# Performance work log

Measured on AMD Instinct MI355X. Metric: run time of the kernel, lower is better.

Reference implementation:

```python
import jax, jax.numpy as jnp
import numpy as np
from jax import lax

KSIZE = 5  # covariance window size

def _avg_pool_same(x):
    # TF avg_pool2d with SAME padding: zero-pad sums, divide by count of VALID (non-pad) elems
    win = (1, KSIZE, KSIZE, 1)
    s = lax.reduce_window(x, 0.0, lax.add, win, (1, 1, 1, 1), 'SAME')
    cnt = lax.reduce_window(jnp.ones((1, x.shape[1], x.shape[2], 1), x.dtype), 0.0, lax.add, win, (1, 1, 1, 1), 'SAME')
    return s / cnt

def _detect_plane_xz(xyz):
    B, H, W, _ = xyz.shape
    P = _avg_pool_same(xyz)                                   # [B,H,W,3] windowed mean
    xyz2 = (xyz[..., :, None] * xyz[..., None, :]).reshape(B, H, W, 9)
    S = _avg_pool_same(xyz2).reshape(B, H, W, 3, 3)            # windowed second moment
    A = S - P[..., :, None] * P[..., None, :]                  # covariance sigma
    A_max = jnp.max(jnp.abs(A), axis=(-2, -1))
    eval_zero = (A_max < 1e-6).astype(xyz.dtype)
    A = A / jnp.maximum(A_max[..., None, None], 1e-6)
    a00, a11, a22 = A[..., 0, 0], A[..., 1, 1], A[..., 2, 2]
    a01, a02, a12 = A[..., 0, 1], A[..., 0, 2], A[..., 1, 2]
    norm = a01 ** 2 + a02 ** 2 + a12 ** 2
    q = (a00 + a11 + a22) / 3.0
    b00, b11, b22 = a00 - q, a11 - q, a22 - q
    p = jnp.sqrt((b00 ** 2 + b11 ** 2 + b22 ** 2 + 2.0 * norm) / 6.0)
    eig_triple = (p < 1e-6).astype(xyz.dtype) * (1.0 - eval_zero)
    c00 = b11 * b22 - a12 * a12
    c01 = a01 * b22 - a12 * a02
    c02 = a01 * a12 - b11 * a02
    det = (b00 * c00 - a01 * c01 + a02 * c02) / jnp.maximum(p, 1e-6) ** 3
    half_det = jnp.clip(0.5 * det, -1.0, 1.0)
    angle = jnp.arccos(half_det) / 3.0
    beta2 = jnp.cos(angle) * 2.0
    beta0 = jnp.cos(angle + np.pi * 2.0 / 3.0) * 2.0
    beta1 = -(beta0 + beta2)
    betas = jnp.stack([beta0, beta1, beta2], axis=-1)
    evals = q[..., None] + p[..., None] * betas
    evals = (eig_triple * q)[..., None] + ((1.0 - eval_zero) * (1.0 - eig_triple))[..., None] * evals
    eval0, eval1, eval2 = evals[..., 0], evals[..., 1], evals[..., 2]
    denom = jnp.sqrt(jnp.maximum((eval0 - eval1) * (eval0 - eval2), 0.0))
    evec_zero = (denom < 1e-6).astype(xyz.dtype)
    ny_num = jnp.sqrt(jnp.maximum(eval0 ** 2 - (a00 + a22) * eval0 + (a00 * a22 - a02 ** 2), 0.0))
    ny = jnp.clip(ny_num / jnp.maximum(denom, 1e-6), 0.0, 1.0)
    return (1.0 - evec_zero) * ny

def _populate_pcd(depth, K):
    B, H, W, _ = depth.shape
    px, py = jnp.meshgrid(jnp.arange(W, dtype=depth.dtype), jnp.arange(H, dtype=depth.dtype))
    grid = jnp.stack([px, py, jnp.ones_like(px)], axis=-1)   # [H,W,3] homogeneous pixels
    xyz = grid[None] * depth                                 # [B,H,W,3]
    K_inv = jnp.linalg.inv(K)
    return jnp.einsum('bij,bhwj->bhwi', K_inv, xyz)

def setup_inputs():
    key = jax.random.key(0)
    B, H, W = 8, 384, 1280
    disp = jax.random.uniform(key, (B, H, W, 1), jnp.float32, 0.005, 0.3)  # normalized disparity
    K0 = jnp.tile(jnp.array([[720.0, 0.0, W / 2.0], [0.0, 720.0, H / 2.0], [0.0, 0.0, 1.0]], jnp.float32)[None], (B, 1, 1))
    baseline = 0.54 * jnp.ones((B,), jnp.float32)
    return {"disp": disp, "K0": K0, "baseline": baseline, "h0": H, "w0": W}

def reference(disp, K0, baseline, h0, w0):
    B, h1, w1, _ = disp.shape
    rw = float(w1) / float(w0)
    rh = float(h1) / float(h0)
    K_scale = jnp.array([[rw, 0.0, 0.5 * (rw - 1.0)], [0.0, rh, 0.5 * (rh - 1.0)], [0.0, 0.0, 1.0]], jnp.float32)
    K1 = K_scale[None] @ K0
    fxb = K1[:, 0, 0] * baseline
    d = float(w1) * jnp.maximum(disp, 1e-6)
    depth = fxb[:, None, None, None] / d
    xyz = _populate_pcd(depth, K1)
    plane_xz = _detect_plane_xz(xyz)
    cond1 = (xyz[..., 1] > 0.3).astype(jnp.float32)
    cond2 = (plane_xz > 0.85).astype(jnp.float32)
    return depth, cond1 * cond2
```

## Files before the change

### kernel.cpp

```cpp
#include <hip/hip_runtime.h>

#define BATCH 8
#define HH 384
#define WW 1280
#define TW 32
#define TH 16
#define NT (TW * TH)
#define LW (TW + 4)
#define LH (TH + 4)

__device__ __forceinline__ float fast_rcp(float x) {
  float r = __builtin_amdgcn_rcpf(x);
  return fmaf(r, fmaf(-x, r, 1.0f), r);
}
__device__ __forceinline__ float fast_sqrt(float x) {
  return __builtin_amdgcn_sqrtf(x);
}
__device__ __forceinline__ float cos_rev(float r) {
  float d;
  asm("v_cos_f32 %0, %1" : "=v"(d) : "v"(r));
  return d;
}

__global__ void prep_kernel(const float* __restrict__ K0,
                            const float* __restrict__ baseline,
                            const int* __restrict__ h0p,
                            const int* __restrict__ w0p,
                            float* __restrict__ cst) {
  int b = threadIdx.x;
  if (b >= BATCH) return;
  float w0 = (float)w0p[0];
  float h0 = (float)h0p[0];
  float rw = (float)WW / w0;
  float rh = (float)HH / h0;
  float s02 = 0.5f * (rw - 1.0f);
  float s12 = 0.5f * (rh - 1.0f);
  const float* K = K0 + b * 9;
  float k0 = rw * K[0] + s02 * K[6];
  float k1 = rw * K[1] + s02 * K[7];
  float k2 = rw * K[2] + s02 * K[8];
  float k3 = rh * K[3] + s12 * K[6];
  float k4 = rh * K[4] + s12 * K[7];
  float k5 = rh * K[5] + s12 * K[8];
  float k6 = K[6], k7 = K[7], k8 = K[8];
  double a = k0, bb = k1, c = k2, d = k3, e = k4, f = k5, g = k6, h = k7, i = k8;
  double cA = e * i - f * h;
  double cB = -(d * i - f * g);
  double cC = d * h - e * g;
  double det = a * cA + bb * cB + c * cC;
  double idet = 1.0 / det;
  float* o = cst + b * 12;
  o[0] = (float)(cA * idet);
  o[1] = (float)(-(bb * i - c * h) * idet);
  o[2] = (float)((bb * f - c * e) * idet);
  o[3] = (float)(cB * idet);
  o[4] = (float)((a * i - c * g) * idet);
  o[5] = (float)(-(a * f - c * d) * idet);
  o[6] = (float)(cC * idet);
  o[7] = (float)(-(a * h - bb * g) * idet);
  o[8] = (float)((a * e - bb * d) * idet);
  o[9] = k0 * baseline[b];
}

__global__ __launch_bounds__(512) void tmap_fused(
    const float* __restrict__ disp,
    const float* __restrict__ cst,
    float* __restrict__ out_depth,
    float* __restrict__ out_mask) {
  __shared__ float4 tile[LH][LW];
  __shared__ float4 vs0[TH][LW];
  __shared__ float4 vs1[TH][LW];
  __shared__ float  vs2[TH][LW];

  const int b = blockIdx.z;
  const float* C = cst + b * 12;
  const float Ki00 = C[0], Ki01 = C[1], Ki02 = C[2];
  const float Ki10 = C[3], Ki11 = C[4], Ki12 = C[5];
  const float Ki20 = C[6], Ki21 = C[7], Ki22 = C[8];
  const float fxb = C[9];

  const int j0 = blockIdx.x * TW;
  const int i0 = blockIdx.y * TH;
  const int tid = threadIdx.y * TW + threadIdx.x;

  for (int s = tid; s < LH * LW; s += NT) {
    const int ti = s / LW;
    const int tj = s - ti * LW;
    const int gi = i0 - 2 + ti;
    const int gj = j0 - 2 + tj;
    float4 v = make_float4(0.0f, 0.0f, 0.0f, 0.0f);
    if (gi >= 0 && gi < HH && gj >= 0 && gj < WW) {
      const float dsp = disp[(b * HH + gi) * WW + gj];
      const float dd = (float)WW * fmaxf(dsp, 1e-6f);
      const float depth = fxb / dd;
      const float jf = (float)gj;
      const float iff = (float)gi;
      v.x = depth * fmaf(Ki00, jf, fmaf(Ki01, iff, Ki02));
      v.y = depth * fmaf(Ki10, jf, fmaf(Ki11, iff, Ki12));
      v.z = depth * fmaf(Ki20, jf, fmaf(Ki21, iff, Ki22));
      v.w = depth;
    }
    tile[ti][tj] = v;
  }
  __syncthreads();

  for (int s = tid; s < TH * LW; s += NT) {
    const int ti = s / LW;
    const int tj = s - ti * LW;
    float sx = 0.f, sy = 0.f, sz = 0.f;
    float sxx = 0.f, sxy = 0.f, sxz = 0.f, syy = 0.f, syz = 0.f, szz = 0.f;
#pragma unroll
    for (int k = 0; k < 5; ++k) {
      const float4 v = tile[ti + k][tj];
      sx += v.x; sy += v.y; sz += v.z;
      sxx = fmaf(v.x, v.x, sxx);
      sxy = fmaf(v.x, v.y, sxy);
      sxz = fmaf(v.x, v.z, sxz);
      syy = fmaf(v.y, v.y, syy);
      syz = fmaf(v.y, v.z, syz);
      szz = fmaf(v.z, v.z, szz);
    }
    vs0[ti][tj] = make_float4(sx, sy, sz, sxx);
    vs1[ti][tj] = make_float4(sxy, sxz, syy, syz);
    vs2[ti][tj] = szz;
  }
  __syncthreads();

  float s1x = 0.f, s1y = 0.f, s1z = 0.f;
  float m00 = 0.f, m01 = 0.f, m02 = 0.f, m11 = 0.f, m12 = 0.f, m22 = 0.f;
#pragma unroll
  for (int w = 0; w < 5; ++w) {
    const float4 va = vs0[threadIdx.y][threadIdx.x + w];
    const float4 vb = vs1[threadIdx.y][threadIdx.x + w];
    const float vc = vs2[threadIdx.y][threadIdx.x + w];
    s1x += va.x; s1y += va.y; s1z += va.z; m00 += va.w;
    m01 += vb.x; m02 += vb.y; m11 += vb.z; m12 += vb.w;
    m22 += vc;
  }

  const int gi = i0 + threadIdx.y;
  const int gj = j0 + threadIdx.x;
  const int ch = min(gi + 2, HH - 1) - max(gi - 2, 0) + 1;
  const int cw = min(gj + 2, WW - 1) - max(gj - 2, 0) + 1;
  const float cnt = (float)(ch * cw);
  const float rcnt = fast_rcp(cnt);

  const float Px = s1x * rcnt, Py = s1y * rcnt, Pz = s1z * rcnt;
  float a00 = m00 * rcnt - Px * Px;
  float a01 = m01 * rcnt - Px * Py;
  float a02 = m02 * rcnt - Px * Pz;
  float a11 = m11 * rcnt - Py * Py;
  float a12 = m12 * rcnt - Py * Pz;
  float a22 = m22 * rcnt - Pz * Pz;

  float Amax = fmaxf(fabsf(a00), fabsf(a11));
  Amax = fmaxf(Amax, fabsf(a22));
  Amax = fmaxf(Amax, fabsf(a01));
  Amax = fmaxf(Amax, fabsf(a02));
  Amax = fmaxf(Amax, fabsf(a12));
  const float eval_zero = (Amax < 1e-6f) ? 1.0f : 0.0f;
  const float rAm = fast_rcp(fmaxf(Amax, 1e-6f));
  a00 *= rAm; a01 *= rAm; a02 *= rAm; a11 *= rAm; a12 *= rAm; a22 *= rAm;

  const float nrm = a01 * a01 + a02 * a02 + a12 * a12;
  const float q = (a00 + a11 + a22) * (1.0f / 3.0f);
  const float b00 = a00 - q, b11 = a11 - q, b22 = a22 - q;
  const float p =
      fast_sqrt((b00 * b00 + b11 * b11 + b22 * b22 + 2.0f * nrm) * (1.0f / 6.0f));
  const float eig_triple = ((p < 1e-6f) ? 1.0f : 0.0f) * (1.0f - eval_zero);
  const float c00 = b11 * b22 - a12 * a12;
  const float c01 = a01 * b22 - a12 * a02;
  const float c02 = a01 * a12 - b11 * a02;
  const float rpm = fast_rcp(fmaxf(p, 1e-6f));
  const float det = (b00 * c00 - a01 * c01 + a02 * c02) * (rpm * rpm * rpm);
  const float half_det = fminf(fmaxf(0.5f * det, -1.0f), 1.0f);
  const float t = acosf(half_det);
  const float rev = t * 0.05305164769729845f;
  const float beta2 = 2.0f * cos_rev(rev);
  const float beta0 = 2.0f * cos_rev(rev + (1.0f / 3.0f));
  const float beta1 = -(beta0 + beta2);
  float e0 = q + p * beta0;
  float e1 = q + p * beta1;
  float e2 = q + p * beta2;
  const float wsel = (1.0f - eval_zero) * (1.0f - eig_triple);
  e0 = eig_triple * q + wsel * e0;
  e1 = eig_triple * q + wsel * e1;
  e2 = eig_triple * q + wsel * e2;

  const float denom = fast_sqrt(fmaxf((e0 - e1) * (e0 - e2), 0.0f));
  const float evec_zero = (denom < 1e-6f) ? 1.0f : 0.0f;
  const float ny_num =
      fast_sqrt(fmaxf(e0 * e0 - (a00 + a22) * e0 + (a00 * a22 - a02 * a02), 0.0f));
  const float ny =
      fminf(fmaxf(ny_num * fast_rcp(fmaxf(denom, 1e-6f)), 0.0f), 1.0f);
  const float plane_xz = (1.0f - evec_zero) * ny;

  const float4 ctr = tile[threadIdx.y + 2][threadIdx.x + 2];
  const float cond1 = (ctr.y > 0.3f) ? 1.0f : 0.0f;
  const float cond2 = (plane_xz > 0.85f) ? 1.0f : 0.0f;

  const int idx = (b * HH + gi) * WW + gj;
  out_depth[idx] = ctr.w;
  out_mask[idx] = cond1 * cond2;
}

extern "C" void kernel_launch(void* const* d_in, const int* in_sizes, int n_in,
                              void* d_out, int out_size, void* d_ws, size_t ws_size,
                              hipStream_t stream) {
  const float* disp = (const float*)d_in[0];
  const float* K0 = (const float*)d_in[1];
  const float* baseline = (const float*)d_in[2];
  const int* h0 = (const int*)d_in[3];
  const int* w0 = (const int*)d_in[4];

  float* cst = (float*)d_ws;
  float* out_depth = (float*)d_out;
  float* out_mask = out_depth + (size_t)BATCH * HH * WW;

  prep_kernel<<<1, BATCH, 0, stream>>>(K0, baseline, h0, w0, cst);

  dim3 block(TW, TH);
  dim3 grid(WW / TW, HH / TH, BATCH);
  tmap_fused<<<grid, block, 0, stream>>>(disp, cst, out_depth, out_mask);
}
```

Before: 117.8 us.

## Halve tile height, add polynomial acos, simplify eigenvalue gap math

Reduces the tile height from 16 to 8 rows, with launch bounds lowered to 256 threads. This raises the halo share of each tile's loaded and recomputed points but may improve occupancy and scheduling. Library acosf is replaced by a Cephes-style polynomial fast_acos, and depth division by a refined hardware reciprocal. The eigenvalue gap product (e0-e1)(e0-e2) is rewritten algebraically in terms of beta0 and beta2 scaled by p, and the Amax reduction is rebalanced into a tree. These trim ALU work but may change rounding near the threshold comparisons.

```diff
diff --git a/kernel.cpp b/kernel.cpp
--- a/kernel.cpp
+++ b/kernel.cpp
@@ -4,7 +4,7 @@
 #define HH 384
 #define WW 1280
 #define TW 32
-#define TH 16
+#define TH 8
 #define NT (TW * TH)
 #define LW (TW + 4)
 #define LH (TH + 4)
@@ -20,6 +20,20 @@
   float d;
   asm("v_cos_f32 %0, %1" : "=v"(d) : "v"(r));
   return d;
+}
+__device__ __forceinline__ float fast_acos(float x) {
+  const float ax = fabsf(x);
+  const bool big = ax > 0.5f;
+  const float z = big ? (1.0f - ax) * 0.5f : x * x;
+  const float u = big ? fast_sqrt(z) : x;
+  float pz = fmaf(z, 4.2163199048e-2f, 2.4181311049e-2f);
+  pz = fmaf(z, pz, 4.5470025998e-2f);
+  pz = fmaf(z, pz, 7.4953002686e-2f);
+  pz = fmaf(z, pz, 1.6666752422e-1f);
+  const float r = fmaf(u * z, pz, u);
+  const float big_res = (x < 0.0f) ? fmaf(-2.0f, r, 3.14159265358979f) : 2.0f * r;
+  const float small_res = 1.57079632679490f - r;
+  return big ? big_res : small_res;
 }
 
 __global__ void prep_kernel(const float* __restrict__ K0,
@@ -62,7 +76,7 @@
   o[9] = k0 * baseline[b];
 }
 
-__global__ __launch_bounds__(512) void tmap_fused(
+__global__ __launch_bounds__(256) void tmap_fused(
     const float* __restrict__ disp,
     const float* __restrict__ cst,
     float* __restrict__ out_depth,
@@ -92,7 +106,7 @@
     if (gi >= 0 && gi < HH && gj >= 0 && gj < WW) {
       const float dsp = disp[(b * HH + gi) * WW + gj];
       const float dd = (float)WW * fmaxf(dsp, 1e-6f);
-      const float depth = fxb / dd;
+      const float depth = fxb * fast_rcp(dd);
       const float jf = (float)gj;
       const float iff = (float)gi;
       v.x = depth * fmaf(Ki00, jf, fmaf(Ki01, iff, Ki02));
@@ -153,11 +167,9 @@
   float a12 = m12 * rcnt - Py * Pz;
   float a22 = m22 * rcnt - Pz * Pz;
 
-  float Amax = fmaxf(fabsf(a00), fabsf(a11));
-  Amax = fmaxf(Amax, fabsf(a22));
-  Amax = fmaxf(Amax, fabsf(a01));
-  Amax = fmaxf(Amax, fabsf(a02));
-  Amax = fmaxf(Amax, fabsf(a12));
+  const float AmA = fmaxf(fmaxf(fabsf(a00), fabsf(a11)), fabsf(a22));
+  const float AmB = fmaxf(fmaxf(fabsf(a01), fabsf(a02)), fabsf(a12));
+  const float Amax = fmaxf(AmA, AmB);
   const float eval_zero = (Amax < 1e-6f) ? 1.0f : 0.0f;
   const float rAm = fast_rcp(fmaxf(Amax, 1e-6f));
   a00 *= rAm; a01 *= rAm; a02 *= rAm; a11 *= rAm; a12 *= rAm; a22 *= rAm;
@@ -174,20 +186,14 @@
   const float rpm = fast_rcp(fmaxf(p, 1e-6f));
   const float det = (b00 * c00 - a01 * c01 + a02 * c02) * (rpm * rpm * rpm);
   const float half_det = fminf(fmaxf(0.5f * det, -1.0f), 1.0f);
-  const float t = acosf(half_det);
+  const float t = fast_acos(half_det);
   const float rev = t * 0.05305164769729845f;
   const float beta2 = 2.0f * cos_rev(rev);
   const float beta0 = 2.0f * cos_rev(rev + (1.0f / 3.0f));
-  const float beta1 = -(beta0 + beta2);
-  float e0 = q + p * beta0;
-  float e1 = q + p * beta1;
-  float e2 = q + p * beta2;
   const float wsel = (1.0f - eval_zero) * (1.0f - eig_triple);
-  e0 = eig_triple * q + wsel * e0;
-  e1 = eig_triple * q + wsel * e1;
-  e2 = eig_triple * q + wsel * e2;
-
-  const float denom = fast_sqrt(fmaxf((e0 - e1) * (e0 - e2), 0.0f));
+  const float e0 = eig_triple * q + wsel * fmaf(p, beta0, q);
+  const float dd2 = (2.0f * beta0 + beta2) * (beta0 - beta2);
+  const float denom = wsel * p * fast_sqrt(fmaxf(dd2, 0.0f));
   const float evec_zero = (denom < 1e-6f) ? 1.0f : 0.0f;
   const float ny_num =
       fast_sqrt(fmaxf(e0 * e0 - (a00 + a22) * e0 + (a00 * a22 - a02 * a02), 0.0f));
```

After: 116.9 us. About the same (-0.8%).
